# Kernel optimization log

Measured on AMD Instinct MI355X. Metric: run time of the kernel, lower is better.

Reference implementation:

```python
import jax, jax.numpy as jnp
import numpy as np

N_EMBD = 1024
N_HEADS = 16
HEAD_SIZE = N_EMBD // N_HEADS
B, T = 2, 2048


def setup_inputs() -> dict:
    key = jax.random.key(0)
    ks = jax.random.split(key, 6)
    s_in = 1.0 / np.sqrt(N_EMBD)
    x = jax.random.normal(ks[0], (B, T, N_EMBD), dtype=jnp.float32)
    # per-head projection weights, stored (H, C, Dh) = x @ W per head
    wq = jax.random.uniform(ks[1], (N_HEADS, N_EMBD, HEAD_SIZE), dtype=jnp.float32, minval=-s_in, maxval=s_in)
    wk = jax.random.uniform(ks[2], (N_HEADS, N_EMBD, HEAD_SIZE), dtype=jnp.float32, minval=-s_in, maxval=s_in)
    wv = jax.random.uniform(ks[3], (N_HEADS, N_EMBD, HEAD_SIZE), dtype=jnp.float32, minval=-s_in, maxval=s_in)
    # output projection (in, out) layout plus bias
    w_proj = jax.random.uniform(ks[4], (N_EMBD, N_EMBD), dtype=jnp.float32, minval=-s_in, maxval=s_in)
    b_proj = jax.random.uniform(ks[5], (N_EMBD,), dtype=jnp.float32, minval=-s_in, maxval=s_in)
    return {"x": x, "wq": wq, "wk": wk, "wv": wv, "w_proj": w_proj, "b_proj": b_proj}


def reference(x, wq, wk, wv, w_proj, b_proj):
    Bb, Tt, C = x.shape
    # all-head QKV projections in one einsum each: (B,T,C)x(H,C,Dh)->(B,H,T,Dh)
    q = jnp.einsum('btc,hcd->bhtd', x, wq)
    k = jnp.einsum('btc,hcd->bhtd', x, wk)
    v = jnp.einsum('btc,hcd->bhtd', x, wv)
    # NOTE: original scales by C**-0.5 with C = full n_embd, not head_size
    scores = jnp.einsum('bhtd,bhsd->bhts', q, k) * (C ** -0.5)
    causal = jnp.tril(jnp.ones((Tt, Tt), dtype=bool))  # is_decoder=True
    scores = jnp.where(causal, scores, -jnp.inf)
    wei = jax.nn.softmax(scores, axis=-1)
    out = jnp.einsum('bhts,bhsd->bhtd', wei, v)
    # concat heads: (B,H,T,Dh) -> (B,T,H*Dh)
    out = out.transpose(0, 2, 1, 3).reshape(Bb, Tt, C)
    return out @ w_proj + b_proj
```

## Files before the change

### kernel.cpp

```cpp
#include <hip/hip_runtime.h>


typedef unsigned short u16;
typedef unsigned int u32;

using bf16x8 = __attribute__((ext_vector_type(8))) short;
using bf16x4 = __attribute__((ext_vector_type(4))) short;
using f32x4  = __attribute__((ext_vector_type(4))) float;

#define T_SEQ 2048
#define C_DIM 1024
#define H_NUM 16
#define D_HEAD 64
#define NCHUNK 40

static __device__ inline f32x4 mfma16(bf16x8 a, bf16x8 b, f32x4 c) {
  return __builtin_amdgcn_mfma_f32_16x16x32_bf16(a, b, c, 0, 0, 0);
}

static __device__ inline short f2bf(float f) {
  union { float f; u32 u; } v; v.f = f;
  u32 u = v.u;
  return (short)((u + 0x7FFFu + ((u >> 16) & 1u)) >> 16);
}

static __device__ inline float bf2f(short s) {
  union { u32 u; float f; } v; v.u = ((u32)(u16)s) << 16;
  return v.f;
}

static __device__ inline float exp2_hw(float x) {
  return __builtin_amdgcn_exp2f(x);
}

static __device__ inline u32 cvtpk_bf16(float a, float b) {
  u32 r;
  asm("v_cvt_pk_bf16_f32 %0, %1, %2" : "=v"(r) : "v"(a), "v"(b));
  return r;
}

static __device__ inline void gload_lds16(const short* g, short* l) {
  __builtin_amdgcn_global_load_lds(
      (const __attribute__((address_space(1))) unsigned int*)g,
      (__attribute__((address_space(3))) unsigned int*)l,
      16, 0, 0);
}

__global__ __launch_bounds__(256) void ingest_kernel(
    const float* __restrict__ x, const float* __restrict__ wq,
    const float* __restrict__ wk, const float* __restrict__ wv,
    const float* __restrict__ wproj,
    short* __restrict__ xb, short* __restrict__ wt, short* __restrict__ wpT) {
  const int bid = blockIdx.x, t = threadIdx.x;
  if (bid < 4096) {
    size_t i4 = ((size_t)bid * 256 + t) * 4;
    const float4 v = *(const float4*)(x + i4);
    bf16x4 o4;
    o4[0] = f2bf(v.x); o4[1] = f2bf(v.y); o4[2] = f2bf(v.z); o4[3] = f2bf(v.w);
    *(bf16x4*)(xb + i4) = o4;
    return;
  }
  __shared__ short lt[64][72];
  const int rl = t >> 2, q16 = (t & 3) * 16;
  if (bid < 4864) {
    const int wb = bid - 4096;
    const int h3 = wb >> 4, c0 = (wb & 15) * 64;
    const float* w = (h3 < 16) ? wq : (h3 < 32) ? wk : wv;
    const int h = h3 & 15;
    const float* rp = w + (size_t)h * 65536 + (size_t)(c0 + rl) * 64 + q16;
#pragma unroll
    for (int j = 0; j < 16; j++) lt[rl][q16 + j] = f2bf(rp[j]);
    __syncthreads();
    short* op = wt + (size_t)h3 * 65536 + (size_t)rl * 1024 + c0 + q16;
#pragma unroll
    for (int j = 0; j < 16; j++) op[j] = lt[q16 + j][rl];
  } else {
    const int wc = bid - 4864;
    const int k0 = (wc >> 4) * 64, n0 = (wc & 15) * 64;
    const float* rp = wproj + (size_t)(k0 + rl) * 1024 + n0 + q16;
#pragma unroll
    for (int j = 0; j < 16; j++) lt[rl][q16 + j] = f2bf(rp[j]);
    __syncthreads();
    short* op = wpT + (size_t)(n0 + rl) * 1024 + k0 + q16;
#pragma unroll
    for (int j = 0; j < 16; j++) op[j] = lt[q16 + j][rl];
  }
}

__global__ __launch_bounds__(256) void qkv_kernel(
    const short* __restrict__ x, const short* __restrict__ wt,
    short* __restrict__ qo, short* __restrict__ ko, short* __restrict__ vto) {
  const int m0 = blockIdx.x * 128;
  const int n0 = blockIdx.y * 128;
  const int tid = threadIdx.x, w = tid >> 6, lane = tid & 63;
  const int l15 = lane & 15, quad = lane >> 4;
  const int wm = w >> 1, wn = w & 1;

  __shared__ __align__(16) short As[2][128 * 32];
  __shared__ __align__(16) short Bs[2][128 * 32];

  const int srow = w * 32 + (lane >> 2);
  const int skof = (lane & 3) * 8;
  const short* ga0 = x  + (size_t)(m0 + srow) * 1024 + skof;
  const short* ga1 = ga0 + 16 * 1024;
  const short* gb0 = wt + (size_t)(n0 + srow) * 1024 + skof;
  const short* gb1 = gb0 + 16 * 1024;
  const int lof0 = (w * 32) * 32;
  const int lof1 = (w * 32 + 16) * 32;

  f32x4 acc[4][4];
#pragma unroll
  for (int i = 0; i < 4; i++)
#pragma unroll
    for (int j = 0; j < 4; j++) acc[i][j] = f32x4{0, 0, 0, 0};

  const bool isv = (n0 >= 2048);

  auto stage = [&](int bi, int kt) {
    const int k0 = kt * 32;
    gload_lds16(ga0 + k0, &As[bi][lof0]);
    gload_lds16(ga1 + k0, &As[bi][lof1]);
    gload_lds16(gb0 + k0, &Bs[bi][lof0]);
    gload_lds16(gb1 + k0, &Bs[bi][lof1]);
  };
  auto compute = [&](int bi) {
    const short* ard = &As[bi][(wm * 64 + l15) * 32 + quad * 8];
    const short* brd = &Bs[bi][(wn * 64 + l15) * 32 + quad * 8];
    bf16x8 af[4], bfr[4];
#pragma unroll
    for (int i = 0; i < 4; i++) {
      af[i]  = *(const bf16x8*)(ard + i * 16 * 32);
      bfr[i] = *(const bf16x8*)(brd + i * 16 * 32);
    }
    if (!isv) {
#pragma unroll
      for (int mi = 0; mi < 4; mi++)
#pragma unroll
        for (int ni = 0; ni < 4; ni++)
          acc[mi][ni] = mfma16(af[mi], bfr[ni], acc[mi][ni]);
    } else {
#pragma unroll
      for (int ni = 0; ni < 4; ni++)
#pragma unroll
        for (int mi = 0; mi < 4; mi++)
          acc[ni][mi] = mfma16(bfr[ni], af[mi], acc[ni][mi]);
    }
  };

  stage(0, 0);
  __syncthreads();
#pragma unroll 1
  for (int kt2 = 0; kt2 < 16; kt2++) {
    stage(1, 2 * kt2 + 1);
    compute(0);
    __syncthreads();
    if (kt2 < 15) stage(0, 2 * kt2 + 2);
    compute(1);
    __syncthreads();
  }

  const int chunk = (n0 >> 6) + wn;
  const int sel = chunk >> 4, h = chunk & 15;
  if (!isv) {
    short* outp = (sel == 0) ? qo : ko;
    const float sc = (sel == 0) ? 0.045084441f : 1.0f;
#pragma unroll
    for (int mi = 0; mi < 4; mi++) {
#pragma unroll
      for (int r = 0; r < 4; r++) {
        int tg = m0 + wm * 64 + mi * 16 + quad * 4 + r;
        int b = tg >> 11, tl = tg & 2047;
        size_t rowb = ((size_t)(b * H_NUM + h) * T_SEQ + tl) * D_HEAD;
#pragma unroll
        for (int ni = 0; ni < 4; ni++)
          outp[rowb + ni * 16 + l15] = f2bf(acc[mi][ni][r] * sc);
      }
    }
  } else {
#pragma unroll
    for (int ni = 0; ni < 4; ni++) {
#pragma unroll
      for (int r = 0; r < 4; r++) {
        int d = ni * 16 + quad * 4 + r;
#pragma unroll
        for (int mi = 0; mi < 4; mi++) {
          int tg = m0 + wm * 64 + mi * 16 + l15;
          int b = tg >> 11, tl = tg & 2047;
          vto[((size_t)(b * H_NUM + h) * D_HEAD + d) * T_SEQ + tl] =
              f2bf(acc[ni][mi][r]);
        }
      }
    }
  }
}

__global__ __launch_bounds__(256) void attn_part_kernel(
    const short* __restrict__ q, const short* __restrict__ k,
    const short* __restrict__ vt, short* __restrict__ po,
    float* __restrict__ pl) {
  static const unsigned char order[NCHUNK] = {
      3, 4, 6, 8, 10, 11, 12, 13, 15, 16, 18, 19, 21, 22, 23, 24, 25, 26,
      28, 29, 30, 32, 33, 34, 36, 37, 38, 39,
      2, 9, 20, 35,
      1, 7, 17, 31,
      0, 5, 14, 27};
  static const unsigned char qtb_of[NCHUNK] = {
      0, 1, 2, 3, 4, 4, 5, 5, 6, 6, 7, 7, 8, 8, 8, 9, 9, 9, 10, 10,
      10, 11, 11, 11, 12, 12, 12, 12, 13, 13, 13, 13, 14, 14, 14, 14,
      15, 15, 15, 15};
  static const unsigned char base16[16] = {0, 1, 2, 3, 4, 6, 8, 10,
                                           12, 15, 18, 21, 24, 28, 32, 36};
  const int id = blockIdx.x;
  const int hb = id & 31;
  const int p  = id >> 5;
  const int pblk = order[p];
  const int qtb = qtb_of[pblk];
  const int sbeg = (pblk - base16[qtb]) * 512;
  const int send = min(sbeg + 512, (qtb + 1) * 128);

  const size_t bh = (size_t)hb;
  const short* qp = q  + bh * T_SEQ * D_HEAD;
  const short* kp = k  + bh * T_SEQ * D_HEAD;
  const short* vp = vt + bh * D_HEAD * T_SEQ;

  const int tid = threadIdx.x;
  const int w4 = tid >> 6;
  const int lane = tid & 63;
  const int l15 = lane & 15, quad = lane >> 4;
  const int swz8 = (l15 & 7) * 8;

  __shared__ __align__(16) short Ks[4096];
  __shared__ __align__(16) short Vs[4096];
  __shared__ __align__(16) short Ps[4][2048];
  short* pp = Ps[w4];

  const int q0w = qtb * 128 + w4 * 32;
  const int s_hi = min(send, ((qtb * 128 + 96 + 95) >> 6) << 6);

  const int srow = w4 * 16 + (lane >> 3);
  const int scol = ((lane & 7) ^ (lane >> 3)) * 8;
  const short* gK0 = kp + (size_t)(sbeg + srow) * 64 + scol;
  const short* gK1 = kp + (size_t)(sbeg + srow + 8) * 64 + scol;
  const short* gV0 = vp + (size_t)srow * 2048 + sbeg + scol;
  const short* gV1 = vp + (size_t)(srow + 8) * 2048 + sbeg + scol;
  short* lK0 = Ks + w4 * 1024 + lane * 8;
  short* lK1 = Ks + w4 * 1024 + 512 + lane * 8;
  short* lV0 = Vs + w4 * 1024 + lane * 8;
  short* lV1 = Vs + w4 * 1024 + 512 + lane * 8;

  auto stageKV = [&](int toff) {
    gload_lds16(gK0 + (size_t)toff * 64, lK0);
    gload_lds16(gK1 + (size_t)toff * 64, lK1);
    gload_lds16(gV0 + toff, lV0);
    gload_lds16(gV1 + toff, lV1);
  };

  const int rbase = l15 * 64;
  const int koff0 = (quad * 8) ^ swz8;
  const int koff1 = (32 + quad * 8) ^ swz8;

  bf16x8 qa[2][2];
#pragma unroll
  for (int h2 = 0; h2 < 2; h2++)
#pragma unroll
    for (int c2 = 0; c2 < 2; c2++)
      qa[h2][c2] = *(const bf16x8*)(qp + (size_t)(q0w + h2 * 16 + l15) * D_HEAD
                                    + c2 * 32 + quad * 8);

  f32x4 o[2][4];
#pragma unroll
  for (int h2 = 0; h2 < 2; h2++)
#pragma unroll
    for (int c = 0; c < 4; c++) o[h2][c] = f32x4{0, 0, 0, 0};
  float l_i[2] = { 0.f, 0.f };

  stageKV(0);

#pragma unroll 1
  for (int s0 = sbeg; s0 < s_hi; s0 += 64) {
    __syncthreads();

    f32x4 s[2][4];
    __builtin_amdgcn_s_setprio(1);
#pragma unroll
    for (int c = 0; c < 4; c++) {
      bf16x8 k0 = *(const bf16x8*)(Ks + c * 1024 + rbase + koff0);
      bf16x8 k1 = *(const bf16x8*)(Ks + c * 1024 + rbase + koff1);
#pragma unroll
      for (int h2 = 0; h2 < 2; h2++) {
        f32x4 z = { 0, 0, 0, 0 };
        z = mfma16(k0, qa[h2][0], z);
        z = mfma16(k1, qa[h2][1], z);
        s[h2][c] = z;
      }
    }
    __builtin_amdgcn_s_setprio(0);

    const bool needMask = (s0 + 64 > q0w);
#pragma unroll
    for (int h2 = 0; h2 < 2; h2++) {
      const int qg = q0w + h2 * 16 + l15;
      if (needMask) {
#pragma unroll
        for (int c = 0; c < 4; c++)
#pragma unroll
          for (int r = 0; r < 4; r++)
            if (s0 + c * 16 + quad * 4 + r > qg) s[h2][c][r] = -1e30f;
      }
      float rs = 0.f;
#pragma unroll
      for (int c = 0; c < 4; c++) {
#pragma unroll
        for (int r = 0; r < 4; r++) {
          float p2 = exp2_hw(s[h2][c][r]);
          s[h2][c][r] = p2;
          rs += p2;
        }
      }
      l_i[h2] += rs;
#pragma unroll
      for (int c = 0; c < 4; c++) {
        uint2 pw;
        pw.x = cvtpk_bf16(s[h2][c][0], s[h2][c][1]);
        pw.y = cvtpk_bf16(s[h2][c][2], s[h2][c][3]);
        *(uint2*)(pp + (h2 * 16 + l15) * 64 + ((c * 16 + quad * 4) ^ swz8)) = pw;
      }
    }
    asm volatile("" ::: "memory");

    __builtin_amdgcn_s_setprio(1);
#pragma unroll
    for (int kb2 = 0; kb2 < 2; kb2++) {
      const int ko = kb2 ? koff1 : koff0;
      bf16x8 pb0 = *(const bf16x8*)(pp + rbase + ko);
      bf16x8 pb1 = *(const bf16x8*)(pp + 1024 + rbase + ko);
#pragma unroll
      for (int c = 0; c < 4; c++) {
        bf16x8 va = *(const bf16x8*)(Vs + c * 1024 + rbase + ko);
        o[0][c] = mfma16(va, pb0, o[0][c]);
        o[1][c] = mfma16(va, pb1, o[1][c]);
      }
    }
    __builtin_amdgcn_s_setprio(0);

    __syncthreads();
    if (s0 + 64 < s_hi) stageKV(s0 + 64 - sbeg);
  }

  const size_t prow = (bh * NCHUNK + pblk) * 128;
#pragma unroll
  for (int h2 = 0; h2 < 2; h2++) {
    float lsum = l_i[h2];
    lsum += __shfl_xor(lsum, 16);
    lsum += __shfl_xor(lsum, 32);
    float inv = (lsum > 0.f) ? 1.0f / lsum : 0.f;
    int qlocal = w4 * 32 + h2 * 16 + l15;
    size_t rowoff = (prow + qlocal) * 64;
#pragma unroll
    for (int c = 0; c < 4; c++) {
      uint2 ow;
      ow.x = cvtpk_bf16(o[h2][c][0] * inv, o[h2][c][1] * inv);
      ow.y = cvtpk_bf16(o[h2][c][2] * inv, o[h2][c][3] * inv);
      *(uint2*)(&po[rowoff + c * 16 + quad * 4]) = ow;
    }
    if (quad == 0) pl[prow + qlocal] = lsum;
  }
}

__global__ __launch_bounds__(256) void attn_merge_kernel(
    const short* __restrict__ po, const float* __restrict__ pl,
    short* __restrict__ attnb) {
  static const unsigned char base16[16] = {0, 1, 2, 3, 4, 6, 8, 10,
                                           12, 15, 18, 21, 24, 28, 32, 36};
  int id = blockIdx.x * 256 + threadIdx.x;
  int dg = id & 7;
  int h  = (id >> 3) & 15;
  int t  = (id >> 7) & 2047;
  int b  = id >> 18;
  int qtb = t >> 7, ql = t & 127;
  int nch = (qtb >> 2) + 1;
  size_t bh = (size_t)(b * H_NUM + h);
  size_t r0 = (bh * NCHUNK + base16[qtb]) * 128 + ql;
  bf16x8 res;
  if (nch == 1) {
    res = *(const bf16x8*)(po + r0 * 64 + dg * 8);
  } else {
    float acc[8] = {0, 0, 0, 0, 0, 0, 0, 0};
    float lsum = 0.f;
    for (int c = 0; c < nch; c++) {
      size_t r = r0 + (size_t)c * 128;
      float lc = pl[r];
      lsum += lc;
      bf16x8 p = *(const bf16x8*)(po + r * 64 + dg * 8);
#pragma unroll
      for (int j = 0; j < 8; j++) acc[j] += lc * bf2f(p[j]);
    }
    float inv = 1.0f / lsum;
#pragma unroll
    for (int j = 0; j < 8; j++) res[j] = f2bf(acc[j] * inv);
  }
  *(bf16x8*)(&attnb[((size_t)(b * T_SEQ + t)) * C_DIM + h * D_HEAD + dg * 8]) = res;
}

__global__ __launch_bounds__(256) void proj_kernel(
    const short* __restrict__ a_in, const short* __restrict__ wpT,
    const float* __restrict__ bias, float* __restrict__ out) {
  const int m0 = blockIdx.x * 128;
  const int n0 = blockIdx.y * 128;
  const int tid = threadIdx.x, w = tid >> 6, lane = tid & 63;
  const int l15 = lane & 15, quad = lane >> 4;
  const int wm = w >> 1, wn = w & 1;

  __shared__ __align__(16) short As[2][128 * 32];
  __shared__ __align__(16) short Bs[2][128 * 32];

  const int srow = w * 32 + (lane >> 2);
  const int skof = (lane & 3) * 8;
  const short* ga0 = a_in + (size_t)(m0 + srow) * 1024 + skof;
  const short* ga1 = ga0 + 16 * 1024;
  const short* gb0 = wpT + (size_t)(n0 + srow) * 1024 + skof;
  const short* gb1 = gb0 + 16 * 1024;
  const int lof0 = (w * 32) * 32;
  const int lof1 = (w * 32 + 16) * 32;

  f32x4 acc[4][4];
#pragma unroll
  for (int i = 0; i < 4; i++)
#pragma unroll
    for (int j = 0; j < 4; j++) acc[i][j] = f32x4{0, 0, 0, 0};

  auto stage = [&](int bi, int kt) {
    const int k0 = kt * 32;
    gload_lds16(ga0 + k0, &As[bi][lof0]);
    gload_lds16(ga1 + k0, &As[bi][lof1]);
    gload_lds16(gb0 + k0, &Bs[bi][lof0]);
    gload_lds16(gb1 + k0, &Bs[bi][lof1]);
  };
  auto compute = [&](int bi) {
    const short* ard = &As[bi][(wm * 64 + l15) * 32 + quad * 8];
    const short* brd = &Bs[bi][(wn * 64 + l15) * 32 + quad * 8];
    bf16x8 af[4], bfr[4];
#pragma unroll
    for (int i = 0; i < 4; i++) {
      af[i]  = *(const bf16x8*)(ard + i * 16 * 32);
      bfr[i] = *(const bf16x8*)(brd + i * 16 * 32);
    }
#pragma unroll
    for (int mi = 0; mi < 4; mi++)
#pragma unroll
      for (int ni = 0; ni < 4; ni++)
        acc[mi][ni] = mfma16(af[mi], bfr[ni], acc[mi][ni]);
  };

  stage(0, 0);
  __syncthreads();
#pragma unroll 1
  for (int kt2 = 0; kt2 < 16; kt2++) {
    stage(1, 2 * kt2 + 1);
    compute(0);
    __syncthreads();
    if (kt2 < 15) stage(0, 2 * kt2 + 2);
    compute(1);
    __syncthreads();
  }

#pragma unroll
  for (int mi = 0; mi < 4; mi++) {
#pragma unroll
    for (int r = 0; r < 4; r++) {
      int mq = m0 + wm * 64 + mi * 16 + quad * 4 + r;
#pragma unroll
      for (int ni = 0; ni < 4; ni++) {
        int n = n0 + wn * 64 + ni * 16 + l15;
        out[(size_t)mq * C_DIM + n] = acc[mi][ni][r] + bias[n];
      }
    }
  }
}

extern "C" void kernel_launch(void* const* d_in, const int* in_sizes, int n_in,
                              void* d_out, int out_size, void* d_ws, size_t ws_size,
                              hipStream_t stream) {
  const float* x     = (const float*)d_in[0];
  const float* wq    = (const float*)d_in[1];
  const float* wk    = (const float*)d_in[2];
  const float* wv    = (const float*)d_in[3];
  const float* wproj = (const float*)d_in[4];
  const float* bias  = (const float*)d_in[5];

  short* ws = (short*)d_ws;
  short* wpT    = ws;
  short* qb     = ws + 1048576;
  short* wt_qkv = ws + 9437184;
  short* xb     = ws + 12582912;
  short* po     = ws + 5242880;
  float* pl     = (float*)(ws + 15728640);
  short* attnb  = ws + 1048576;
  short* kb     = (short*)d_out;
  short* vtb    = (short*)d_out + 4194304;

  ingest_kernel<<<5120, 256, 0, stream>>>(x, wq, wk, wv, wproj, xb, wt_qkv, wpT);
  qkv_kernel<<<dim3(32, 24), 256, 0, stream>>>(xb, wt_qkv, qb, kb, vtb);
  attn_part_kernel<<<NCHUNK * 32, 256, 0, stream>>>(qb, kb, vtb, po, pl);
  attn_merge_kernel<<<2048, 256, 0, stream>>>(po, pl, attnb);
  proj_kernel<<<dim3(32, 8), 256, 0, stream>>>(attnb, wpT, bias, (float*)d_out);
}
```

Measured before the change: 196.4 us.

## Double-buffer K/V tiles in LDS to overlap loads with compute

Splits the K and V shared-memory tiles into two buffers. Each iteration now issues the global-to-LDS load for the next tile before computing on the current one, so load latency can hide behind the MFMA work. The loop is unrolled by two, and the causal upper bound comes from the chunk extent rather than the separate s_hi clamp. The extra buffers raise LDS use per block, which may cut how many blocks fit on each compute unit.

```diff
diff --git a/kernel.cpp b/kernel.cpp
--- a/kernel.cpp
+++ b/kernel.cpp
@@ -229,13 +229,13 @@
   const int l15 = lane & 15, quad = lane >> 4;
   const int swz8 = (l15 & 7) * 8;
 
-  __shared__ __align__(16) short Ks[4096];
-  __shared__ __align__(16) short Vs[4096];
+  __shared__ __align__(16) short Ks[2][4096];
+  __shared__ __align__(16) short Vs[2][4096];
   __shared__ __align__(16) short Ps[4][2048];
   short* pp = Ps[w4];
 
   const int q0w = qtb * 128 + w4 * 32;
-  const int s_hi = min(send, ((qtb * 128 + 96 + 95) >> 6) << 6);
+  const int iters = (send - sbeg) >> 6;
 
   const int srow = w4 * 16 + (lane >> 3);
   const int scol = ((lane & 7) ^ (lane >> 3)) * 8;
@@ -243,16 +243,13 @@
   const short* gK1 = kp + (size_t)(sbeg + srow + 8) * 64 + scol;
   const short* gV0 = vp + (size_t)srow * 2048 + sbeg + scol;
   const short* gV1 = vp + (size_t)(srow + 8) * 2048 + sbeg + scol;
-  short* lK0 = Ks + w4 * 1024 + lane * 8;
-  short* lK1 = Ks + w4 * 1024 + 512 + lane * 8;
-  short* lV0 = Vs + w4 * 1024 + lane * 8;
-  short* lV1 = Vs + w4 * 1024 + 512 + lane * 8;
-
-  auto stageKV = [&](int toff) {
-    gload_lds16(gK0 + (size_t)toff * 64, lK0);
-    gload_lds16(gK1 + (size_t)toff * 64, lK1);
-    gload_lds16(gV0 + toff, lV0);
-    gload_lds16(gV1 + toff, lV1);
+  const int lofs = w4 * 1024 + lane * 8;
+
+  auto stageKV = [&](short* Kb, short* Vb, int toff) {
+    gload_lds16(gK0 + (size_t)toff * 64, Kb + lofs);
+    gload_lds16(gK1 + (size_t)toff * 64, Kb + lofs + 512);
+    gload_lds16(gV0 + toff, Vb + lofs);
+    gload_lds16(gV1 + toff, Vb + lofs + 512);
   };
 
   const int rbase = l15 * 64;
@@ -274,18 +271,13 @@
     for (int c = 0; c < 4; c++) o[h2][c] = f32x4{0, 0, 0, 0};
   float l_i[2] = { 0.f, 0.f };
 
-  stageKV(0);
-
-#pragma unroll 1
-  for (int s0 = sbeg; s0 < s_hi; s0 += 64) {
-    __syncthreads();
-
+  auto computeTile = [&](const short* Kb, const short* Vb, int s0) {
     f32x4 s[2][4];
     __builtin_amdgcn_s_setprio(1);
 #pragma unroll
     for (int c = 0; c < 4; c++) {
-      bf16x8 k0 = *(const bf16x8*)(Ks + c * 1024 + rbase + koff0);
-      bf16x8 k1 = *(const bf16x8*)(Ks + c * 1024 + rbase + koff1);
+      bf16x8 k0 = *(const bf16x8*)(Kb + c * 1024 + rbase + koff0);
+      bf16x8 k1 = *(const bf16x8*)(Kb + c * 1024 + rbase + koff1);
 #pragma unroll
       for (int h2 = 0; h2 < 2; h2++) {
         f32x4 z = { 0, 0, 0, 0 };
@@ -336,15 +328,25 @@
       bf16x8 pb1 = *(const bf16x8*)(pp + 1024 + rbase + ko);
 #pragma unroll
       for (int c = 0; c < 4; c++) {
-        bf16x8 va = *(const bf16x8*)(Vs + c * 1024 + rbase + ko);
+        bf16x8 va = *(const bf16x8*)(Vb + c * 1024 + rbase + ko);
         o[0][c] = mfma16(va, pb0, o[0][c]);
         o[1][c] = mfma16(va, pb1, o[1][c]);
       }
     }
     __builtin_amdgcn_s_setprio(0);
-
-    __syncthreads();
-    if (s0 + 64 < s_hi) stageKV(s0 + 64 - sbeg);
+    asm volatile("" ::: "memory");
+  };
+
+  stageKV(Ks[0], Vs[0], 0);
+  __syncthreads();
+#pragma unroll 1
+  for (int t = 0; t < iters; t += 2) {
+    stageKV(Ks[1], Vs[1], (t + 1) * 64);
+    computeTile(Ks[0], Vs[0], sbeg + t * 64);
+    __syncthreads();
+    if (t + 2 < iters) stageKV(Ks[0], Vs[0], (t + 2) * 64);
+    computeTile(Ks[1], Vs[1], sbeg + (t + 1) * 64);
+    __syncthreads();
   }
 
   const size_t prow = (bh * NCHUNK + pblk) * 128;
```

After: 197.4 us. No clear change (+0.5%).
